# Kernel optimization log

Measured on AMD Instinct MI355X. Metric: run time of the kernel, lower is better.

Reference implementation:

```python
import jax, jax.numpy as jnp
import numpy as np

K_IN = 25      # prod(kernel)
H_LEN = 128    # hidden_length


def setup_inputs() -> dict:
    key = jax.random.key(0)
    ks = jax.random.split(key, 7)
    B, S, R = 16, 128, 1024
    in_dim = K_IN + H_LEN + 1  # 154
    mid = 256
    # fan-in scaled init (like torch Linear default scale ~1/sqrt(fan_in))
    x = jax.random.normal(ks[0], (B, S, R, K_IN), dtype=jnp.float32)
    hidden = jax.random.normal(ks[1], (B, R, H_LEN), dtype=jnp.float32)
    cost = jax.random.normal(ks[2], (B, S), dtype=jnp.float32)
    Wo1 = jax.random.normal(ks[3], (in_dim, mid), dtype=jnp.float32) / np.sqrt(in_dim)
    Wo2 = jax.random.normal(ks[4], (mid, 1), dtype=jnp.float32) / np.sqrt(mid)
    Wh1 = jax.random.normal(ks[5], (in_dim, mid), dtype=jnp.float32) / np.sqrt(in_dim)
    Wh2 = jax.random.normal(ks[6], (mid, H_LEN), dtype=jnp.float32) / np.sqrt(mid)
    return {"x": x, "hidden": hidden, "cost": cost,
            "Wo1": Wo1, "Wo2": Wo2, "Wh1": Wh1, "Wh2": Wh2}


def reference(x, hidden, cost, Wo1, Wo2, Wh1, Wh2):
    # x: [B,S,R,K]  hidden: [B,R,H]  cost: [B,S]
    B, S, R, K = x.shape

    def step(h, inp):
        xs, cs = inp  # xs: [B,R,K], cs: [B]
        c = jnp.broadcast_to(cs[:, None, None], (B, R, 1))
        inter = jnp.concatenate([xs, h, c], axis=-1)        # [B,R,K+H+1]
        out = ((inter @ Wo1) @ Wo2)[..., 0]                 # i2o: [B,R]
        h_new = (inter @ Wh1) @ Wh2                         # i2h: [B,R,H]
        return h_new, out

    xs_seq = jnp.swapaxes(x, 0, 1)       # [S,B,R,K]
    cost_seq = jnp.swapaxes(cost, 0, 1)  # [S,B]
    h_final, outs = jax.lax.scan(step, hidden, (xs_seq, cost_seq))
    return jnp.swapaxes(outs, 0, 1), h_final  # ([B,S,R], [B,R,H])
```

## Files before the change

kernel.cpp:

```cpp
#include <hip/hip_runtime.h>

#define B_   16
#define S_   128
#define R_   1024
#define KIN  25
#define H_   128
#define MID  256
#define KP   160

typedef _Float16 h8 __attribute__((ext_vector_type(8)));
typedef _Float16 h2 __attribute__((ext_vector_type(2)));
typedef float    f4v __attribute__((ext_vector_type(4)));

__device__ __forceinline__ h2 pk2(float a, float b) {
    auto r = __builtin_amdgcn_cvt_pkrtz(a, b);
    h2 o; o[0] = (_Float16)r[0]; o[1] = (_Float16)r[1]; return o;
}
__device__ __forceinline__ unsigned h2u(h2 v) {
    union { h2 h; unsigned u; } c; c.h = v; return c.u;
}
__device__ __forceinline__ h8 mk8(unsigned a, unsigned b, unsigned c, unsigned d) {
    union { h8 v; unsigned u[4]; } r; r.u[0] = a; r.u[1] = b; r.u[2] = c; r.u[3] = d;
    return r.v;
}

__device__ __forceinline__ int orig_k(int kp) {
    if (kp < H_)        return KIN + kp;
    if (kp < H_ + KIN)  return kp - H_;
    if (kp == H_ + KIN) return H_ + KIN;
    return -1;
}

__global__ void prep_kernel(const float* __restrict__ Wo1, const float* __restrict__ Wo2,
                            const float* __restrict__ Wh1, const float* __restrict__ Wh2,
                            _Float16* __restrict__ WTP, _Float16* __restrict__ woP)
{
    const int kp = blockIdx.x;
    const int t  = threadIdx.x;
    if (kp < KP) {
        const int ok = orig_k(kp);
        float acc = 0.f;
        if (ok >= 0) {
            const float* w1 = Wh1 + (long)ok * MID;
            for (int m = 0; m < MID; ++m)
                acc += w1[m] * Wh2[m * H_ + t];
        }
        WTP[t * KP + kp] = (_Float16)acc;
    } else {
#pragma unroll
        for (int r = 0; r < 2; ++r) {
            int k2 = t + r * 128;
            if (k2 < KP) {
                int ok = orig_k(k2);
                float acc = 0.f;
                if (ok >= 0)
                    for (int m = 0; m < MID; ++m)
                        acc += Wo1[ok * MID + m] * Wo2[m];
                woP[k2] = (_Float16)acc;
            }
        }
    }
}

__global__ __launch_bounds__(64, 1) void rnn_main(
    const float* __restrict__ x, const float* __restrict__ hidden,
    const float* __restrict__ cost, const _Float16* __restrict__ WTP,
    const _Float16* __restrict__ woP, float* __restrict__ outs,
    float* __restrict__ hfin)
{
    __shared__ float costS[136];

    const int t = threadIdx.x;
    const int c = t & 15, g = t >> 4;
    const int b  = blockIdx.x >> 6;
    const int r0 = (blockIdx.x & 63) << 4;

    h8 af[8][5];
#pragma unroll
    for (int it = 0; it < 8; ++it)
#pragma unroll
        for (int kb = 0; kb < 5; ++kb)
            af[it][kb] = *reinterpret_cast<const h8*>(
                &WTP[(it * 16 + c) * KP + kb * 32 + g * 8]);
    h8 wz;
#pragma unroll
    for (int u = 0; u < 8; ++u) wz[u] = (_Float16)0.f;
    h8 afo[5];
#pragma unroll
    for (int kb = 0; kb < 5; ++kb) {
        h8 w = *reinterpret_cast<const h8*>(&woP[kb * 32 + g * 8]);
        afo[kb] = (c == 0) ? w : wz;
    }

    costS[t]      = cost[b * S_ + t];
    costS[t + 64] = cost[b * S_ + t + 64];
    if (t < 8) costS[128 + t] = 0.f;

    h8 bf[4];
    {
        const float* hp = hidden + ((long)(b * R_ + r0 + c)) * H_;
#pragma unroll
        for (int kb = 0; kb < 4; ++kb) {
            float4 v0 = *reinterpret_cast<const float4*>(hp + kb * 32 + g * 8);
            float4 v1 = *reinterpret_cast<const float4*>(hp + kb * 32 + g * 8 + 4);
            bf[kb] = mk8(h2u(pk2(v0.x, v0.y)), h2u(pk2(v0.z, v0.w)),
                         h2u(pk2(v1.x, v1.y)), h2u(pk2(v1.z, v1.w)));
        }
    }

    const int xoff  = (g == 3) ? 21 : g * 8;
    const int xoff2 = (g == 3) ? 0 : 4;
    const float* xlane = x + (((long)b * S_) * R_ + r0 + c) * KIN + xoff;

    float4 X0a, X0b, X1a, X1b, X2a, X2b, X3a, X3b;
    auto xinit = [&](int s, float4& v0, float4& v1) {
        const float* p = xlane + (long)s * (R_ * KIN);
        v0 = *reinterpret_cast<const float4*>(p);
        v1 = *reinterpret_cast<const float4*>(p + xoff2);
    };
    xinit(0, X0a, X0b); xinit(1, X1a, X1b); xinit(2, X2a, X2b); xinit(3, X3a, X3b);

    auto mkbx = [&](float4 v0, float4 v1, float cs) -> h8 {
        h2 z{};
        h2 d0 = (g == 3) ? pk2(v0.w, cs) : pk2(v0.x, v0.y);
        h2 d1 = (g == 3) ? z : pk2(v0.z, v0.w);
        h2 d2 = (g == 3) ? z : pk2(v1.x, v1.y);
        h2 d3 = (g == 3) ? z : pk2(v1.z, v1.w);
        return mk8(h2u(d0), h2u(d1), h2u(d2), h2u(d3));
    };

    const f4v fz = {0.f, 0.f, 0.f, 0.f};
    f4v acc[8], acco = fz;
    float4 ccA = *reinterpret_cast<const float4*>(&costS[0]);
    float4 ccB;

#define STEP(SV, XV0, XV1, CSV, OG) do {                                        \
    h8 bx = mkbx(XV0, XV1, CSV);                                                \
    if ((SV) + 4 < S_) {                                                        \
        const float* p_ = xlane + (long)((SV) + 4) * (R_ * KIN);                \
        XV0 = *reinterpret_cast<const float4*>(p_);                             \
        XV1 = *reinterpret_cast<const float4*>(p_ + xoff2);                     \
    }                                                                           \
    _Pragma("unroll")                                                           \
    for (int kb = 0; kb < 5; ++kb) {                                            \
        h8 bv = (kb < 4) ? bf[kb] : bx;                                         \
        _Pragma("unroll")                                                       \
        for (int it = 0; it < 8; ++it)                                          \
            acc[it] = __builtin_amdgcn_mfma_f32_16x16x32_f16(                   \
                af[it][kb], bv, kb == 0 ? fz : acc[it], 0, 0, 0);               \
        acco = __builtin_amdgcn_mfma_f32_16x16x32_f16(                          \
            afo[kb], bv, kb == 0 ? fz : acco, 0, 0, 0);                         \
    }                                                                           \
    OG = acco[0];                       \
    if ((SV) < S_ - 1) {                                                        \
        _Pragma("unroll")                                                       \
        for (int kb = 0; kb < 4; ++kb) {                                        \
            unsigned A0 = h2u(pk2(acc[2*kb][0],   acc[2*kb][1]));               \
            unsigned A1 = h2u(pk2(acc[2*kb][2],   acc[2*kb][3]));               \
            unsigned B0 = h2u(pk2(acc[2*kb+1][0], acc[2*kb+1][1]));             \
            unsigned B1 = h2u(pk2(acc[2*kb+1][2], acc[2*kb+1][3]));             \
            auto r0_ = __builtin_amdgcn_permlane32_swap(A0, B0, false, false);  \
            auto q0_ = __builtin_amdgcn_permlane16_swap(r0_[0], r0_[1], false, false); \
            auto r1_ = __builtin_amdgcn_permlane32_swap(A1, B1, false, false);  \
            auto q1_ = __builtin_amdgcn_permlane16_swap(r1_[0], r1_[1], false, false); \
            bf[kb] = mk8(q0_[0], q1_[0], q0_[1], q1_[1]);                       \
        }                                                                       \
    }                                                                           \
} while (0)

    for (int s4 = 0; s4 < S_; s4 += 8) {
        float og0, og1, og2, og3;
        ccB = *reinterpret_cast<const float4*>(&costS[s4 + 4]);
        STEP(s4 + 0, X0a, X0b, ccA[0], og0);
        STEP(s4 + 1, X1a, X1b, ccA[1], og1);
        STEP(s4 + 2, X2a, X2b, ccA[2], og2);
        STEP(s4 + 3, X3a, X3b, ccA[3], og3);
        if (g == 0) {
            float* op = outs + (long)(b * S_ + s4) * R_ + r0 + c;
            op[0] = og0; op[R_] = og1; op[2 * R_] = og2; op[3 * R_] = og3;
        }
        ccA = *reinterpret_cast<const float4*>(&costS[s4 + 8]);
        STEP(s4 + 4, X0a, X0b, ccB[0], og0);
        STEP(s4 + 5, X1a, X1b, ccB[1], og1);
        STEP(s4 + 6, X2a, X2b, ccB[2], og2);
        STEP(s4 + 7, X3a, X3b, ccB[3], og3);
        if (g == 0) {
            float* op = outs + (long)(b * S_ + s4 + 4) * R_ + r0 + c;
            op[0] = og0; op[R_] = og1; op[2 * R_] = og2; op[3 * R_] = og3;
        }
    }
#undef STEP

#pragma unroll
    for (int it = 0; it < 8; ++it)
        *reinterpret_cast<f4v*>(
            &hfin[((long)(b * R_ + r0 + c)) * H_ + it * 16 + g * 4]) = acc[it];
}

extern "C" void kernel_launch(void* const* d_in, const int* in_sizes, int n_in,
                              void* d_out, int out_size, void* d_ws, size_t ws_size,
                              hipStream_t stream)
{
    const float* x      = (const float*)d_in[0];
    const float* hidden = (const float*)d_in[1];
    const float* cost   = (const float*)d_in[2];
    const float* Wo1    = (const float*)d_in[3];
    const float* Wo2    = (const float*)d_in[4];
    const float* Wh1    = (const float*)d_in[5];
    const float* Wh2    = (const float*)d_in[6];

    float* outs = (float*)d_out;
    float* hfin = outs + (long)B_ * S_ * R_;

    _Float16* WTP = (_Float16*)d_ws;
    _Float16* woP = WTP + (size_t)H_ * KP;

    prep_kernel<<<KP + 1, 128, 0, stream>>>(Wo1, Wo2, Wh1, Wh2, WTP, woP);
    rnn_main<<<1024, 64, 0, stream>>>(x, hidden, cost, WTP, woP, outs, hfin);
}
```

Before: 92.48 us.

## Unroll recurrence by four steps using precomputed powers of hidden weight matrix

The linear recurrence is rewritten so that each iteration advances four timesteps at once. It uses precomputed W^4 for the hidden term, along with per-offset x-projection matrices (W^0..W^3 applied to the input weights) and output vectors. This removes the per-step serial dependency chain of MFMA, pack and permute. Each 4-step block then costs 8 chained MFMA k-blocks instead of 20, with fewer fp16 round-trips of the hidden state. In exchange there are six small prep kernels, more register-resident fragments, and error from fp16 matrix powers that may grow differently.

Result: slower. 108.4 us (+17.2%).

```diff
diff --git a/kernel.cpp b/kernel.cpp
--- a/kernel.cpp
+++ b/kernel.cpp
@@ -6,7 +6,6 @@
 #define KIN  25
 #define H_   128
 #define MID  256
-#define KP   160
 
 typedef _Float16 h8 __attribute__((ext_vector_type(8)));
 typedef _Float16 h2 __attribute__((ext_vector_type(2)));
@@ -24,48 +23,114 @@
     return r.v;
 }
 
-__device__ __forceinline__ int orig_k(int kp) {
-    if (kp < H_)        return KIN + kp;
-    if (kp < H_ + KIN)  return kp - H_;
-    if (kp == H_ + KIN) return H_ + KIN;
-    return -1;
-}
-
-__global__ void prep_kernel(const float* __restrict__ Wo1, const float* __restrict__ Wo2,
-                            const float* __restrict__ Wh1, const float* __restrict__ Wh2,
-                            _Float16* __restrict__ WTP, _Float16* __restrict__ woP)
-{
-    const int kp = blockIdx.x;
-    const int t  = threadIdx.x;
-    if (kp < KP) {
-        const int ok = orig_k(kp);
-        float acc = 0.f;
-        if (ok >= 0) {
-            const float* w1 = Wh1 + (long)ok * MID;
-            for (int m = 0; m < MID; ++m)
-                acc += w1[m] * Wh2[m * H_ + t];
-        }
-        WTP[t * KP + kp] = (_Float16)acc;
+__global__ void prepA(const float* __restrict__ Wh1, const float* __restrict__ Wh2,
+                      const float* __restrict__ Wo1, const float* __restrict__ Wo2,
+                      float* __restrict__ Wc, float* __restrict__ wo)
+{
+    const int k = blockIdx.x, t = threadIdx.x;
+    if (k < 154) {
+        float a = 0.f;
+        for (int m = 0; m < MID; ++m) a += Wh1[k * MID + m] * Wh2[m * H_ + t];
+        Wc[k * H_ + t] = a;
     } else {
 #pragma unroll
         for (int r = 0; r < 2; ++r) {
-            int k2 = t + r * 128;
-            if (k2 < KP) {
-                int ok = orig_k(k2);
-                float acc = 0.f;
-                if (ok >= 0)
-                    for (int m = 0; m < MID; ++m)
-                        acc += Wo1[ok * MID + m] * Wo2[m];
-                woP[k2] = (_Float16)acc;
+            int kk = t + r * 128;
+            if (kk < 154) {
+                float a = 0.f;
+                for (int m = 0; m < MID; ++m) a += Wo1[kk * MID + m] * Wo2[m];
+                wo[kk] = a;
             }
         }
+    }
+}
+__global__ void prepB(const float* __restrict__ Wc, float* __restrict__ M2)
+{
+    const int i = blockIdx.x, t = threadIdx.x;
+    float a = 0.f;
+    for (int q = 0; q < H_; ++q) a += Wc[(25 + i) * H_ + q] * Wc[(25 + q) * H_ + t];
+    M2[i * H_ + t] = a;
+}
+__global__ void prepC(const float* __restrict__ Wc, const float* __restrict__ M2,
+                      float* __restrict__ M3)
+{
+    const int i = blockIdx.x, t = threadIdx.x;
+    float a = 0.f;
+    for (int q = 0; q < H_; ++q) a += M2[i * H_ + q] * Wc[(25 + q) * H_ + t];
+    M3[i * H_ + t] = a;
+}
+__global__ void prepD(const float* __restrict__ M2, _Float16* __restrict__ W4h)
+{
+    const int i = blockIdx.x, t = threadIdx.x;
+    float a = 0.f;
+    for (int q = 0; q < H_; ++q) a += M2[t * H_ + q] * M2[q * H_ + i];
+    W4h[i * H_ + t] = (_Float16)a;
+}
+__global__ void prepE1(const float* __restrict__ Wc, const float* __restrict__ wo,
+                       const float* __restrict__ M2, const float* __restrict__ M3,
+                       float* __restrict__ vf, _Float16* __restrict__ VV)
+{
+    const int i = threadIdx.x;
+    float v0 = wo[25 + i], v1 = 0.f, v2 = 0.f, v3 = 0.f;
+    for (int q = 0; q < H_; ++q) {
+        float wh = wo[25 + q];
+        v1 += Wc[(25 + i) * H_ + q] * wh;
+        v2 += M2[i * H_ + q] * wh;
+        v3 += M3[i * H_ + q] * wh;
+    }
+    vf[0 * H_ + i] = v0; vf[1 * H_ + i] = v1; vf[2 * H_ + i] = v2; vf[3 * H_ + i] = v3;
+    VV[0 * H_ + i] = (_Float16)v0; VV[1 * H_ + i] = (_Float16)v1;
+    VV[2 * H_ + i] = (_Float16)v2; VV[3 * H_ + i] = (_Float16)v3;
+    for (int r = 4; r < 16; ++r) VV[r * H_ + i] = (_Float16)0.f;
+}
+__global__ void prepE2(const float* __restrict__ Wc, const float* __restrict__ wo,
+                       const float* __restrict__ M2, const float* __restrict__ M3,
+                       const float* __restrict__ vf,
+                       _Float16* __restrict__ XWst, _Float16* __restrict__ OXT)
+{
+    const int p = threadIdx.x;
+    if (blockIdx.x < 128) {
+        const int i = blockIdx.x;
+        float x0 = 0.f, x1 = 0.f, x2 = 0.f, x3 = 0.f;
+        if (p < 26) {
+            const int kp = (p < 25) ? p : 153;
+            x0 = Wc[kp * H_ + i];
+            for (int q = 0; q < H_; ++q) {
+                float wx = Wc[kp * H_ + q];
+                x1 += wx * Wc[(25 + q) * H_ + i];
+                x2 += wx * M2[q * H_ + i];
+                x3 += wx * M3[q * H_ + i];
+            }
+        }
+        XWst[(0 * H_ + i) * 32 + p] = (_Float16)x0;
+        XWst[(1 * H_ + i) * 32 + p] = (_Float16)x1;
+        XWst[(2 * H_ + i) * 32 + p] = (_Float16)x2;
+        XWst[(3 * H_ + i) * 32 + p] = (_Float16)x3;
+    } else {
+        float w0 = 0.f, w1 = 0.f, w2 = 0.f, w3 = 0.f;
+        if (p < 26) {
+            const int kp = (p < 25) ? p : 153;
+            w0 = wo[kp];
+            for (int q = 0; q < H_; ++q) {
+                float wx = Wc[kp * H_ + q];
+                w1 += wx * vf[0 * H_ + q];
+                w2 += wx * vf[1 * H_ + q];
+                w3 += wx * vf[2 * H_ + q];
+            }
+        }
+        float wa[4] = {w0, w1, w2, w3};
+        for (int j = 0; j < 4; ++j)
+            for (int r = 0; r < 16; ++r)
+                OXT[(j * 16 + r) * 32 + p] =
+                    (r >= j && r - j < 4) ? (_Float16)wa[r - j] : (_Float16)0.f;
     }
 }
 
 __global__ __launch_bounds__(64, 1) void rnn_main(
     const float* __restrict__ x, const float* __restrict__ hidden,
-    const float* __restrict__ cost, const _Float16* __restrict__ WTP,
-    const _Float16* __restrict__ woP, float* __restrict__ outs,
+    const float* __restrict__ cost, const _Float16* __restrict__ W4h,
+    const _Float16* __restrict__ XWst, const _Float16* __restrict__ VV,
+    const _Float16* __restrict__ OXT, float* __restrict__ outs,
     float* __restrict__ hfin)
 {
     __shared__ float costS[136];
@@ -75,37 +140,46 @@
     const int b  = blockIdx.x >> 6;
     const int r0 = (blockIdx.x & 63) << 4;
 
-    h8 af[8][5];
+    h8 w4f[8][4];
 #pragma unroll
     for (int it = 0; it < 8; ++it)
 #pragma unroll
-        for (int kb = 0; kb < 5; ++kb)
-            af[it][kb] = *reinterpret_cast<const h8*>(
-                &WTP[(it * 16 + c) * KP + kb * 32 + g * 8]);
-    h8 wz;
-#pragma unroll
-    for (int u = 0; u < 8; ++u) wz[u] = (_Float16)0.f;
-    h8 afo[5];
-#pragma unroll
-    for (int kb = 0; kb < 5; ++kb) {
-        h8 w = *reinterpret_cast<const h8*>(&woP[kb * 32 + g * 8]);
-        afo[kb] = (c == 0) ? w : wz;
-    }
+        for (int kb = 0; kb < 4; ++kb)
+            w4f[it][kb] = *reinterpret_cast<const h8*>(
+                &W4h[(it * 16 + c) * H_ + kb * 32 + g * 8]);
+    h8 xw0f[8], xw1f[8], xw2f[8], xw3f[8];
+#pragma unroll
+    for (int it = 0; it < 8; ++it) {
+        xw0f[it] = *reinterpret_cast<const h8*>(&XWst[(0 * H_ + it * 16 + c) * 32 + g * 8]);
+        xw1f[it] = *reinterpret_cast<const h8*>(&XWst[(1 * H_ + it * 16 + c) * 32 + g * 8]);
+        xw2f[it] = *reinterpret_cast<const h8*>(&XWst[(2 * H_ + it * 16 + c) * 32 + g * 8]);
+        xw3f[it] = *reinterpret_cast<const h8*>(&XWst[(3 * H_ + it * 16 + c) * 32 + g * 8]);
+    }
+    h8 ohf[4];
+#pragma unroll
+    for (int kb = 0; kb < 4; ++kb)
+        ohf[kb] = *reinterpret_cast<const h8*>(&VV[c * H_ + kb * 32 + g * 8]);
+    h8 oxf0, oxf1, oxf2, oxf3;
+    oxf0 = *reinterpret_cast<const h8*>(&OXT[(0 * 16 + c) * 32 + g * 8]);
+    oxf1 = *reinterpret_cast<const h8*>(&OXT[(1 * 16 + c) * 32 + g * 8]);
+    oxf2 = *reinterpret_cast<const h8*>(&OXT[(2 * 16 + c) * 32 + g * 8]);
+    oxf3 = *reinterpret_cast<const h8*>(&OXT[(3 * 16 + c) * 32 + g * 8]);
 
     costS[t]      = cost[b * S_ + t];
     costS[t + 64] = cost[b * S_ + t + 64];
     if (t < 8) costS[128 + t] = 0.f;
 
-    h8 bf[4];
+    h8 bf0, bf1, bf2, bf3;
     {
         const float* hp = hidden + ((long)(b * R_ + r0 + c)) * H_;
-#pragma unroll
-        for (int kb = 0; kb < 4; ++kb) {
-            float4 v0 = *reinterpret_cast<const float4*>(hp + kb * 32 + g * 8);
-            float4 v1 = *reinterpret_cast<const float4*>(hp + kb * 32 + g * 8 + 4);
-            bf[kb] = mk8(h2u(pk2(v0.x, v0.y)), h2u(pk2(v0.z, v0.w)),
-                         h2u(pk2(v1.x, v1.y)), h2u(pk2(v1.z, v1.w)));
-        }
+        float4 v0, v1;
+#define LDH(KB, DST)                                                            \
+        v0 = *reinterpret_cast<const float4*>(hp + (KB) * 32 + g * 8);          \
+        v1 = *reinterpret_cast<const float4*>(hp + (KB) * 32 + g * 8 + 4);      \
+        DST = mk8(h2u(pk2(v0.x, v0.y)), h2u(pk2(v0.z, v0.w)),                   \
+                  h2u(pk2(v1.x, v1.y)), h2u(pk2(v1.z, v1.w)));
+        LDH(0, bf0) LDH(1, bf1) LDH(2, bf2) LDH(3, bf3)
+#undef LDH
     }
 
     const int xoff  = (g == 3) ? 21 : g * 8;
@@ -113,12 +187,11 @@
     const float* xlane = x + (((long)b * S_) * R_ + r0 + c) * KIN + xoff;
 
     float4 X0a, X0b, X1a, X1b, X2a, X2b, X3a, X3b;
-    auto xinit = [&](int s, float4& v0, float4& v1) {
-        const float* p = xlane + (long)s * (R_ * KIN);
-        v0 = *reinterpret_cast<const float4*>(p);
-        v1 = *reinterpret_cast<const float4*>(p + xoff2);
-    };
-    xinit(0, X0a, X0b); xinit(1, X1a, X1b); xinit(2, X2a, X2b); xinit(3, X3a, X3b);
+#define XLD(S, VA, VB) {                                                        \
+        const float* p_ = xlane + (long)(S) * (R_ * KIN);                       \
+        VA = *reinterpret_cast<const float4*>(p_);                              \
+        VB = *reinterpret_cast<const float4*>(p_ + xoff2); }
+    XLD(0, X0a, X0b) XLD(1, X1a, X1b) XLD(2, X2a, X2b) XLD(3, X3a, X3b)
 
     auto mkbx = [&](float4 v0, float4 v1, float cs) -> h8 {
         h2 z{};
@@ -129,67 +202,77 @@
         return mk8(h2u(d0), h2u(d1), h2u(d2), h2u(d3));
     };
 
+    float4 cc = *reinterpret_cast<const float4*>(&costS[0]);
+    h8 bx0 = mkbx(X0a, X0b, cc.x), bx1 = mkbx(X1a, X1b, cc.y);
+    h8 bx2 = mkbx(X2a, X2b, cc.z), bx3 = mkbx(X3a, X3b, cc.w);
+
     const f4v fz = {0.f, 0.f, 0.f, 0.f};
-    f4v acc[8], acco = fz;
-    float4 ccA = *reinterpret_cast<const float4*>(&costS[0]);
-    float4 ccB;
-
-#define STEP(SV, XV0, XV1, CSV, OG) do {                                        \
-    h8 bx = mkbx(XV0, XV1, CSV);                                                \
-    if ((SV) + 4 < S_) {                                                        \
-        const float* p_ = xlane + (long)((SV) + 4) * (R_ * KIN);                \
-        XV0 = *reinterpret_cast<const float4*>(p_);                             \
-        XV1 = *reinterpret_cast<const float4*>(p_ + xoff2);                     \
-    }                                                                           \
-    _Pragma("unroll")                                                           \
-    for (int kb = 0; kb < 5; ++kb) {                                            \
-        h8 bv = (kb < 4) ? bf[kb] : bx;                                         \
-        _Pragma("unroll")                                                       \
-        for (int it = 0; it < 8; ++it)                                          \
-            acc[it] = __builtin_amdgcn_mfma_f32_16x16x32_f16(                   \
-                af[it][kb], bv, kb == 0 ? fz : acc[it], 0, 0, 0);               \
-        acco = __builtin_amdgcn_mfma_f32_16x16x32_f16(                          \
-            afo[kb], bv, kb == 0 ? fz : acco, 0, 0, 0);                         \
-    }                                                                           \
-    OG = acco[0];                       \
-    if ((SV) < S_ - 1) {                                                        \
-        _Pragma("unroll")                                                       \
-        for (int kb = 0; kb < 4; ++kb) {                                        \
-            unsigned A0 = h2u(pk2(acc[2*kb][0],   acc[2*kb][1]));               \
-            unsigned A1 = h2u(pk2(acc[2*kb][2],   acc[2*kb][3]));               \
-            unsigned B0 = h2u(pk2(acc[2*kb+1][0], acc[2*kb+1][1]));             \
-            unsigned B1 = h2u(pk2(acc[2*kb+1][2], acc[2*kb+1][3]));             \
-            auto r0_ = __builtin_amdgcn_permlane32_swap(A0, B0, false, false);  \
-            auto q0_ = __builtin_amdgcn_permlane16_swap(r0_[0], r0_[1], false, false); \
-            auto r1_ = __builtin_amdgcn_permlane32_swap(A1, B1, false, false);  \
-            auto q1_ = __builtin_amdgcn_permlane16_swap(r1_[0], r1_[1], false, false); \
-            bf[kb] = mk8(q0_[0], q1_[0], q0_[1], q1_[1]);                       \
-        }                                                                       \
-    }                                                                           \
+    f4v acc[8], acco;
+
+#define MM(AF, BV, CV) __builtin_amdgcn_mfma_f32_16x16x32_f16((AF), (BV), (CV), 0, 0, 0)
+#define TAIL(AE, AO, DST) do {                                                  \
+    unsigned A0 = h2u(pk2((AE)[0], (AE)[1]));                                   \
+    unsigned A1 = h2u(pk2((AE)[2], (AE)[3]));                                   \
+    unsigned B0 = h2u(pk2((AO)[0], (AO)[1]));                                   \
+    unsigned B1 = h2u(pk2((AO)[2], (AO)[3]));                                   \
+    auto r0_ = __builtin_amdgcn_permlane32_swap(A0, B0, false, false);          \
+    auto q0_ = __builtin_amdgcn_permlane16_swap(r0_[0], r0_[1], false, false);  \
+    auto r1_ = __builtin_amdgcn_permlane32_swap(A1, B1, false, false);          \
+    auto q1_ = __builtin_amdgcn_permlane16_swap(r1_[0], r1_[1], false, false);  \
+    DST = mk8(q0_[0], q1_[0], q0_[1], q1_[1]);                                  \
 } while (0)
 
-    for (int s4 = 0; s4 < S_; s4 += 8) {
-        float og0, og1, og2, og3;
-        ccB = *reinterpret_cast<const float4*>(&costS[s4 + 4]);
-        STEP(s4 + 0, X0a, X0b, ccA[0], og0);
-        STEP(s4 + 1, X1a, X1b, ccA[1], og1);
-        STEP(s4 + 2, X2a, X2b, ccA[2], og2);
-        STEP(s4 + 3, X3a, X3b, ccA[3], og3);
+    for (int s4 = 0; s4 < S_; s4 += 4) {
+        {
+            const int sn = (s4 + 4) & (S_ - 1);
+            XLD(sn,     X0a, X0b) XLD(sn + 1, X1a, X1b)
+            XLD(sn + 2, X2a, X2b) XLD(sn + 3, X3a, X3b)
+        }
+        acco = MM(oxf0, bx0, fz);
+#pragma unroll
+        for (int it = 0; it < 8; ++it) acc[it] = MM(xw3f[it], bx0, fz);
+        acco = MM(oxf1, bx1, acco);
+#pragma unroll
+        for (int it = 0; it < 8; ++it) acc[it] = MM(xw2f[it], bx1, acc[it]);
+        acco = MM(oxf2, bx2, acco);
+#pragma unroll
+        for (int it = 0; it < 8; ++it) acc[it] = MM(xw1f[it], bx2, acc[it]);
+        acco = MM(oxf3, bx3, acco);
+#pragma unroll
+        for (int it = 0; it < 8; ++it) acc[it] = MM(xw0f[it], bx3, acc[it]);
+        acco = MM(ohf[0], bf0, acco);
+#pragma unroll
+        for (int it = 0; it < 8; ++it) acc[it] = MM(w4f[it][0], bf0, acc[it]);
+        acco = MM(ohf[1], bf1, acco);
+#pragma unroll
+        for (int it = 0; it < 8; ++it) acc[it] = MM(w4f[it][1], bf1, acc[it]);
+        acco = MM(ohf[2], bf2, acco);
+#pragma unroll
+        for (int it = 0; it < 8; ++it) acc[it] = MM(w4f[it][2], bf2, acc[it]);
+        acco = MM(ohf[3], bf3, acco);
+#pragma unroll
+        for (int it = 0; it < 8; ++it) acc[it] = MM(w4f[it][3], bf3, acc[it]);
+
         if (g == 0) {
             float* op = outs + (long)(b * S_ + s4) * R_ + r0 + c;
-            op[0] = og0; op[R_] = og1; op[2 * R_] = og2; op[3 * R_] = og3;
-        }
-        ccA = *reinterpret_cast<const float4*>(&costS[s4 + 8]);
-        STEP(s4 + 4, X0a, X0b, ccB[0], og0);
-        STEP(s4 + 5, X1a, X1b, ccB[1], og1);
-        STEP(s4 + 6, X2a, X2b, ccB[2], og2);
-        STEP(s4 + 7, X3a, X3b, ccB[3], og3);
-        if (g == 0) {
-            float* op = outs + (long)(b * S_ + s4 + 4) * R_ + r0 + c;
-            op[0] = og0; op[R_] = og1; op[2 * R_] = og2; op[3 * R_] = og3;
-        }
-    }
-#undef STEP
+            op[0]      = acco[0];
+            op[R_]     = acco[1];
+            op[2 * R_] = acco[2];
+            op[3 * R_] = acco[3];
+        }
+        TAIL(acc[0], acc[1], bf0);
+        TAIL(acc[2], acc[3], bf1);
+        TAIL(acc[4], acc[5], bf2);
+        TAIL(acc[6], acc[7], bf3);
+        float4 ccn = *reinterpret_cast<const float4*>(&costS[s4 + 4]);
+        bx0 = mkbx(X0a, X0b, ccn.x);
+        bx1 = mkbx(X1a, X1b, ccn.y);
+        bx2 = mkbx(X2a, X2b, ccn.z);
+        bx3 = mkbx(X3a, X3b, ccn.w);
+    }
+#undef TAIL
+#undef MM
+#undef XLD
 
 #pragma unroll
     for (int it = 0; it < 8; ++it)
@@ -212,9 +295,22 @@
     float* outs = (float*)d_out;
     float* hfin = outs + (long)B_ * S_ * R_;
 
-    _Float16* WTP = (_Float16*)d_ws;
-    _Float16* woP = WTP + (size_t)H_ * KP;
-
-    prep_kernel<<<KP + 1, 128, 0, stream>>>(Wo1, Wo2, Wh1, Wh2, WTP, woP);
-    rnn_main<<<1024, 64, 0, stream>>>(x, hidden, cost, WTP, woP, outs, hfin);
-}
+    char* wsb = (char*)d_ws;
+    float*    Wc   = (float*)wsb;                       wsb += 154 * H_ * 4;
+    float*    wo   = (float*)wsb;                       wsb += 160 * 4;
+    float*    M2   = (float*)wsb;                       wsb += H_ * H_ * 4;
+    float*    M3   = (float*)wsb;                       wsb += H_ * H_ * 4;
+    float*    vf   = (float*)wsb;                       wsb += 4 * H_ * 4;
+    _Float16* W4h  = (_Float16*)wsb;                    wsb += H_ * H_ * 2;
+    _Float16* XWst = (_Float16*)wsb;                    wsb += 4 * H_ * 32 * 2;
+    _Float16* VV   = (_Float16*)wsb;                    wsb += 16 * H_ * 2;
+    _Float16* OXT  = (_Float16*)wsb;                    wsb += 4 * 16 * 32 * 2;
+
+    prepA<<<155, 128, 0, stream>>>(Wh1, Wh2, Wo1, Wo2, Wc, wo);
+    prepB<<<128, 128, 0, stream>>>(Wc, M2);
+    prepC<<<128, 128, 0, stream>>>(Wc, M2, M3);
+    prepD<<<128, 128, 0, stream>>>(M2, W4h);
+    prepE1<<<1, 128, 0, stream>>>(Wc, wo, M2, M3, vf, VV);
+    prepE2<<<129, 32, 0, stream>>>(Wc, wo, M2, M3, vf, XWst, OXT);
+    rnn_main<<<1024, 64, 0, stream>>>(x, hidden, cost, W4h, XWst, VV, OXT, outs, hfin);
+}
```
